# Kernel optimization log

Hardware: AMD Instinct MI355X
Metric: run time of the kernel (lower is better)

Reference implementation:

```python
import jax, jax.numpy as jnp
import numpy as np

D_MODEL = 1024
N_HEAD = 16
L, B = 2048, 2


def setup_inputs() -> dict:
    key = jax.random.key(0)
    ks = jax.random.split(key, 11)
    inp = {
        "q": jax.random.normal(ks[0], (L, B, D_MODEL), dtype=jnp.float32),
        "k": jax.random.normal(ks[1], (L, B, D_MODEL), dtype=jnp.float32),
        "v": jax.random.normal(ks[2], (L, B, D_MODEL), dtype=jnp.float32),
        "sph": jax.random.uniform(ks[3], (B, N_HEAD, L, L), dtype=jnp.float32),
        "mask": jax.random.randint(ks[4], (B, L, L), 0, 2, dtype=jnp.int32),
        # learned params (torch Linear stores W of shape [out, in]; y = x @ W.T)
        "Wq": jax.random.normal(ks[5], (D_MODEL, D_MODEL), dtype=jnp.float32) * (1.0 / np.sqrt(D_MODEL)),
        "Wk": jax.random.normal(ks[6], (D_MODEL, D_MODEL), dtype=jnp.float32) * (1.0 / np.sqrt(D_MODEL)),
        "Wv": jax.random.normal(ks[7], (D_MODEL, D_MODEL), dtype=jnp.float32) * (1.0 / np.sqrt(D_MODEL)),
        "Wfc": jax.random.normal(ks[8], (D_MODEL, D_MODEL), dtype=jnp.float32) * (1.0 / np.sqrt(D_MODEL)),
        "gamma": jnp.ones((D_MODEL,), dtype=jnp.float32),
        "beta": jnp.zeros((D_MODEL,), dtype=jnp.float32),
    }
    return inp


def reference(q, k, v, sph, mask, Wq, Wk, Wv, Wfc, gamma, beta):
    # q, k, v: [L, B, D]  ->  batch-first [B, L, D]
    n_head = N_HEAD
    Lq, Bb, D = q.shape
    d_k = D // n_head
    x_q = jnp.transpose(q, (1, 0, 2))
    x_k = jnp.transpose(k, (1, 0, 2))
    x_v = jnp.transpose(v, (1, 0, 2))
    residual = x_q  # [B, L, D]

    # projections (no bias), split heads: [B, H, L, d_k]
    qh = (x_q @ Wq.T).reshape(Bb, Lq, n_head, d_k).transpose(0, 2, 1, 3)
    kh = (x_k @ Wk.T).reshape(Bb, Lq, n_head, d_k).transpose(0, 2, 1, 3)
    vh = (x_v @ Wv.T).reshape(Bb, Lq, n_head, d_k).transpose(0, 2, 1, 3)

    scale = jnp.asarray(d_k, qh.dtype) ** 0.5
    attn = jnp.einsum('bhqd,bhkd->bhqk', qh / scale, kh)
    attn = attn * sph                                   # spatial decay modulation
    attn = jnp.where(mask[:, None, :, :] == 0, jnp.asarray(-1e9, attn.dtype), attn)
    p_attn = jax.nn.softmax(attn, axis=-1)              # dropout is identity in eval

    out = jnp.einsum('bhqk,bhkd->bhqd', p_attn, vh)     # [B, H, L, d_k]
    out = out.transpose(0, 2, 1, 3).reshape(Bb, Lq, D)
    out = out @ Wfc.T + residual                        # fc (no bias) + residual

    # LayerNorm(eps=1e-6)
    mu = jnp.mean(out, axis=-1, keepdims=True)
    var = jnp.var(out, axis=-1, keepdims=True)
    out = (out - mu) * jax.lax.rsqrt(var + 1e-6) * gamma + beta

    return jnp.transpose(out, (1, 0, 2)), p_attn
```

## Files before the change

kernel.cpp:

```cpp
#include <hip/hip_runtime.h>
#include <hip/hip_bf16.h>

#define LL 2048
#define BB 2
#define DD 1024
#define HH 16
#define DKk 64

typedef __attribute__((ext_vector_type(8))) short s8v;
typedef __attribute__((ext_vector_type(8))) unsigned short u8v;
typedef __attribute__((ext_vector_type(4))) float f4v;

__device__ __forceinline__ ushort f2b(float f){
  union { __hip_bfloat16 h; ushort u; } c; c.h = __float2bfloat16(f); return c.u;
}
__device__ __forceinline__ float b2f(ushort u){
  union { __hip_bfloat16 h; ushort u; } c; c.u = u; return __bfloat162float(c.h);
}
__device__ __forceinline__ void nts4(float* p, f4v v){ __builtin_nontemporal_store(v, (f4v*)p); }

__global__ __launch_bounds__(256) void pack_all_kernel(
    const float* __restrict__ q, const float* __restrict__ k, const float* __restrict__ v,
    const float* __restrict__ Wq, const float* __restrict__ Wk,
    const float* __restrict__ Wv, const float* __restrict__ Wfc,
    const int* __restrict__ mask,
    ushort* __restrict__ xq, ushort* __restrict__ xk, ushort* __restrict__ xv,
    ushort* __restrict__ wb, unsigned* __restrict__ mbits2){
  int blk = blockIdx.x;
  if (blk < 2048){
    int t = blk*256 + threadIdx.x;
    int m = t >> 7;
    int dc = (t & 127) << 3;
    int b = m >> 11, l = m & (LL-1);
    size_t src = ((size_t)(l*BB + b) << 10) + dc;
    size_t dst = ((size_t)m << 10) + dc;
    #pragma unroll
    for (int i=0;i<3;++i){
      const float* ss = (i==0)?q:(i==1)?k:v;
      ushort* dd = (i==0)?xq:(i==1)?xk:xv;
      float4 a = *(const float4*)(ss+src);
      float4 bb = *(const float4*)(ss+src+4);
      u8v o;
      o[0]=f2b(a.x); o[1]=f2b(a.y); o[2]=f2b(a.z); o[3]=f2b(a.w);
      o[4]=f2b(bb.x);o[5]=f2b(bb.y);o[6]=f2b(bb.z);o[7]=f2b(bb.w);
      *(u8v*)(dd+dst) = o;
    }
  } else if (blk < 4096){
    int t = (blk-2048)*256 + threadIdx.x;
    int which = t >> 17;
    size_t idx = (size_t)(t & 131071) << 3;
    const float* s = (which==0)?Wq:(which==1)?Wk:(which==2)?Wv:Wfc;
    float4 a = *(const float4*)(s+idx);
    float4 b4 = *(const float4*)(s+idx+4);
    u8v o;
    o[0]=f2b(a.x);o[1]=f2b(a.y);o[2]=f2b(a.z);o[3]=f2b(a.w);
    o[4]=f2b(b4.x);o[5]=f2b(b4.y);o[6]=f2b(b4.z);o[7]=f2b(b4.w);
    *(u8v*)(wb + ((size_t)which<<20) + idx) = o;
  } else {
    int t = (blk-4096)*256 + threadIdx.x;
    int rowg = t >> 6, lane = t & 63;
    const int* mrow = mask + ((size_t)rowg<<11) + (lane<<2);
    unsigned mw = 0;
    #pragma unroll
    for (int ct=0; ct<8; ++ct){
      int4 a = *(const int4*)(mrow + (ct<<8));
      unsigned nib = (a.x&1) | ((a.y&1)<<1) | ((a.z&1)<<2) | ((a.w&1)<<3);
      mw |= nib << (ct*4);
    }
    mbits2[((size_t)rowg<<6) + lane] = mw;
  }
}

__device__ __forceinline__ void gemm_body(
    const ushort* __restrict__ A, const ushort* __restrict__ W,
    ushort* __restrict__ outb, float* __restrict__ outf, const float* __restrict__ resid,
    int mode, float scale){
  __shared__ ushort As[4096];
  __shared__ ushort Bs[4096];
  int tid = threadIdx.x;
  int w = tid>>6, lane = tid&63, lane15 = lane&15, g = lane>>4;
  int m0 = blockIdx.y<<7, n0 = blockIdx.x<<7;
  int wr = w>>1, wc = w&1;
  f4v z4 = {0.f,0.f,0.f,0.f};
  f4v acc[4][4];
  #pragma unroll
  for (int i=0;i<4;++i)
    #pragma unroll
    for (int j=0;j<4;++j) acc[i][j] = z4;

  int f0 = tid, f1 = 256 + tid;
  int r0 = f0>>2, c0 = (f0&3)<<3;
  int r1 = f1>>2, c1 = (f1&3)<<3;
  for (int k0=0; k0<1024; k0+=32){
    *(s8v*)&As[(r0<<5)+c0] = *(const s8v*)&A[((size_t)(m0+r0)<<10) + k0 + c0];
    *(s8v*)&As[(r1<<5)+c1] = *(const s8v*)&A[((size_t)(m0+r1)<<10) + k0 + c1];
    *(s8v*)&Bs[(r0<<5)+c0] = *(const s8v*)&W[((size_t)(n0+r0)<<10) + k0 + c0];
    *(s8v*)&Bs[(r1<<5)+c1] = *(const s8v*)&W[((size_t)(n0+r1)<<10) + k0 + c1];
    __syncthreads();
    s8v af[4], bf_[4];
    #pragma unroll
    for (int mi=0;mi<4;++mi) af[mi] = *(s8v*)&As[((wr*64 + mi*16 + lane15)<<5) + (g<<3)];
    #pragma unroll
    for (int ni=0;ni<4;++ni) bf_[ni] = *(s8v*)&Bs[((wc*64 + ni*16 + lane15)<<5) + (g<<3)];
    #pragma unroll
    for (int mi=0;mi<4;++mi)
      #pragma unroll
      for (int ni=0;ni<4;++ni)
        acc[mi][ni] = __builtin_amdgcn_mfma_f32_16x16x32_bf16(af[mi], bf_[ni], acc[mi][ni], 0,0,0);
    __syncthreads();
  }
  #pragma unroll
  for (int mi=0;mi<4;++mi){
    #pragma unroll
    for (int ni=0;ni<4;++ni){
      int mbase = m0 + wr*64 + mi*16 + (g<<2);
      int ncol  = n0 + wc*64 + ni*16 + lane15;
      if (mode==0){
        int b=mbase>>11, h=ncol>>6, j=ncol&63;
        size_t o = (((size_t)(b*HH+h)*LL + (mbase&2047))<<6) + j;
        #pragma unroll
        for (int r=0;r<4;++r) outb[o + ((size_t)r<<6)] = f2b(acc[mi][ni][r]*scale);
      } else if (mode==2){
        int b=mbase>>11, h=ncol>>6, j=ncol&63;
        ushort4 pk = make_ushort4(f2b(acc[mi][ni][0]), f2b(acc[mi][ni][1]),
                                  f2b(acc[mi][ni][2]), f2b(acc[mi][ni][3]));
        *(ushort4*)&outb[(((size_t)(b*HH+h)*DKk + j)<<11) + (mbase&2047)] = pk;
      } else {
        int b=mbase>>11, l2=mbase&2047;
        #pragma unroll
        for (int r=0;r<4;++r)
          outf[((size_t)(mbase+r)<<10)+ncol] =
              acc[mi][ni][r] + resid[((size_t)((l2+r)*BB + b)<<10) + ncol];
      }
    }
  }
}

__global__ __launch_bounds__(256) void gemm_qkv_kernel(
    const ushort* __restrict__ xq, const ushort* __restrict__ xk, const ushort* __restrict__ xv,
    const ushort* __restrict__ wb, ushort* __restrict__ Qh, ushort* __restrict__ Kh, ushort* __restrict__ Vt){
  int z = blockIdx.z;
  const ushort* A = (z==0)?xq:(z==1)?xk:xv;
  const ushort* W = wb + ((size_t)z<<20);
  ushort* outb = (z==0)?Qh:(z==1)?Kh:Vt;
  int mode = (z==2)?2:0;
  float scale = (z==0)?0.125f:1.0f;
  gemm_body(A, W, outb, nullptr, nullptr, mode, scale);
}

__global__ __launch_bounds__(256) void gemm_fc_kernel(
    const ushort* __restrict__ ao, const ushort* __restrict__ wfc,
    const float* __restrict__ resid, float* __restrict__ fco){
  gemm_body(ao, wfc, nullptr, fco, resid, 3, 1.0f);
}

__global__ __launch_bounds__(1024, 4) void attn_kernel(
    const ushort* __restrict__ Qh, const ushort* __restrict__ Kh, const ushort* __restrict__ Vt,
    const float* __restrict__ sph, const unsigned* __restrict__ mbits2,
    float* __restrict__ p_out, ushort* __restrict__ attn_out){
  extern __shared__ char smem[];
  float* pbuf   = (float*)(smem + 16384);
  float* redsum = (float*)(smem + 16384 + 13056);
  int tid = threadIdx.x, w = tid>>6, lane = tid&63, lane15 = lane&15, g = lane>>4;
  int bid = blockIdx.x;
  int qt = bid & 127, h = (bid>>7)&15, b = bid>>11;
  int q0 = qt<<4;
  size_t bh = (size_t)b*HH + h;
  int qrow = q0 + w;

  const float* sph_r = sph + ((bh*LL + qrow)<<11) + (lane<<2);
  unsigned mw = mbits2[(((size_t)b*LL + qrow)<<6) + lane];

  const ushort* Qbase = Qh + ((bh*LL + q0 + lane15)<<6) + (g<<3);
  s8v qa0 = *(const s8v*)Qbase;
  s8v qa1 = *(const s8v*)(Qbase + 32);

  int rswz = (w&7)<<4;
  int aswz = (lane15&7)<<4;
  int ds = w & 3, kg = w >> 2;
  float sum = 0.f;
  f4v sp0, sp1;
  ushort4 ev[8];
  f4v oacc = {0.f,0.f,0.f,0.f};

  asm volatile("global_load_dwordx4 %0, %1, off" : "=v"(sp0) : "v"(sph_r));

  #pragma unroll
  for (int ct=0; ct<8; ++ct){
    if (ct<7){
      const float* pn = sph_r + ((ct+1)<<8);
      if (ct&1) asm volatile("global_load_dwordx4 %0, %1, off" : "=v"(sp0) : "v"(pn));
      else      asm volatile("global_load_dwordx4 %0, %1, off" : "=v"(sp1) : "v"(pn));
    }

    const ushort* Kp = Kh + ((bh*LL + (ct<<8) + (w<<4) + lane15)<<6) + (g<<3);
    s8v kb0 = *(const s8v*)Kp;
    s8v kb1 = *(const s8v*)(Kp + 32);
    f4v cacc = {0.f,0.f,0.f,0.f};
    cacc = __builtin_amdgcn_mfma_f32_16x16x32_bf16(qa0, kb0, cacc, 0,0,0);
    cacc = __builtin_amdgcn_mfma_f32_16x16x32_bf16(qa1, kb1, cacc, 0,0,0);
    char* Sb = smem + ((ct&1)<<13);
    int colb = ((w<<4) + lane15)<<1;
    #pragma unroll
    for (int r=0;r<4;++r){
      int ri = (g<<2)+r;
      *(ushort*)(Sb + (ri<<9) + (colb ^ ((ri&7)<<4))) = f2b(cacc[r]);
    }
    __syncthreads();

    f4v spv;
    if (ct&1){ asm volatile("s_waitcnt vmcnt(0)" : "+v"(sp1)); spv = sp1; }
    else     { asm volatile("s_waitcnt vmcnt(0)" : "+v"(sp0)); spv = sp0; }
    __builtin_amdgcn_sched_barrier(0);

    char* Srow = Sb + (w<<9);
    int boff = (lane<<3) ^ rswz;
    ushort4 sv = *(ushort4*)(Srow + boff);
    unsigned m4 = mw >> (ct*4);
    float e0 = (m4&1) ? __expf(b2f(sv.x)*spv[0]) : 0.f;
    float e1 = (m4&2) ? __expf(b2f(sv.y)*spv[1]) : 0.f;
    float e2 = (m4&4) ? __expf(b2f(sv.z)*spv[2]) : 0.f;
    float e3 = (m4&8) ? __expf(b2f(sv.w)*spv[3]) : 0.f;
    sum += (e0+e1)+(e2+e3);
    ushort4 eb = make_ushort4(f2b(e0), f2b(e1), f2b(e2), f2b(e3));
    ev[ct] = eb;
    *(ushort4*)(Srow + boff) = eb;
    __syncthreads();

    const ushort* Vb = Vt + ((bh*DKk + (ds<<4) + lane15)<<11) + (ct<<8) + (kg<<6) + (g<<3);
    s8v vb0 = *(const s8v*)Vb;
    s8v vb1 = *(const s8v*)(Vb + 32);
    char* Sa = Sb + (lane15<<9);
    s8v pa0 = *(s8v*)(Sa + (((kg<<7) + (g<<4)) ^ aswz));
    s8v pa1 = *(s8v*)(Sa + (((kg<<7) + 64 + (g<<4)) ^ aswz));
    oacc = __builtin_amdgcn_mfma_f32_16x16x32_bf16(pa0, vb0, oacc, 0,0,0);
    oacc = __builtin_amdgcn_mfma_f32_16x16x32_bf16(pa1, vb1, oacc, 0,0,0);
  }

  #pragma unroll
  for (int off=1; off<64; off<<=1) sum += __shfl_xor(sum, off, 64);
  if (lane==0) redsum[w] = sum;
  float inv = 1.0f / sum;
  float* prow = p_out + ((bh*LL + qrow)<<11) + (lane<<2);
  #pragma unroll
  for (int ct=0;ct<8;++ct){
    f4v o;
    o[0]=b2f(ev[ct].x)*inv; o[1]=b2f(ev[ct].y)*inv;
    o[2]=b2f(ev[ct].z)*inv; o[3]=b2f(ev[ct].w)*inv;
    nts4(prow + (ct<<8), o);
  }

  if (kg){
    float* pp = pbuf + (kg-1)*1088;
    #pragma unroll
    for (int r=0;r<4;++r) pp[((g<<2)+r)*68 + (ds<<4) + lane15] = oacc[r];
  }
  __syncthreads();
  if (kg==0){
    #pragma unroll
    for (int p3=0;p3<3;++p3){
      float* pp = pbuf + p3*1088;
      #pragma unroll
      for (int r=0;r<4;++r) oacc[r] += pp[((g<<2)+r)*68 + (ds<<4) + lane15];
    }
    #pragma unroll
    for (int r=0;r<4;++r){
      int qr = (g<<2)+r;
      float val = oacc[r] / redsum[qr];
      attn_out[((size_t)(b*LL + q0 + qr)<<10) + (h<<6) + (ds<<4) + lane15] = f2b(val);
    }
  }
}

__global__ __launch_bounds__(256) void ln_kernel(const float* __restrict__ fc,
    const float* __restrict__ gamma, const float* __restrict__ beta, float* __restrict__ out){
  __shared__ float rs[4], rq[4];
  int m = blockIdx.x, tid = threadIdx.x;
  int d0 = tid<<2;
  float4 x = *(const float4*)(fc + ((size_t)m<<10) + d0);
  float s = x.x+x.y+x.z+x.w;
  float sq = x.x*x.x+x.y*x.y+x.z*x.z+x.w*x.w;
  #pragma unroll
  for (int off=32; off; off>>=1){ s += __shfl_xor(s,off,64); sq += __shfl_xor(sq,off,64); }
  if ((tid&63)==0){ rs[tid>>6]=s; rq[tid>>6]=sq; }
  __syncthreads();
  float ts = rs[0]+rs[1]+rs[2]+rs[3];
  float tq = rq[0]+rq[1]+rq[2]+rq[3];
  float mu = ts*(1.0f/1024.0f);
  float var = tq*(1.0f/1024.0f) - mu*mu;
  float rr = rsqrtf(var + 1e-6f);
  float4 gm = *(const float4*)(gamma + d0);
  float4 bt = *(const float4*)(beta + d0);
  float4 y;
  y.x=(x.x-mu)*rr*gm.x+bt.x;
  y.y=(x.y-mu)*rr*gm.y+bt.y;
  y.z=(x.z-mu)*rr*gm.z+bt.z;
  y.w=(x.w-mu)*rr*gm.w+bt.w;
  int b=m>>11, l2=m&2047;
  *(float4*)(out + ((size_t)(l2*BB+b)<<10) + d0) = y;
}

extern "C" void kernel_launch(void* const* d_in, const int* in_sizes, int n_in,
                              void* d_out, int out_size, void* d_ws, size_t ws_size,
                              hipStream_t stream){
  const float* q    = (const float*)d_in[0];
  const float* k    = (const float*)d_in[1];
  const float* v    = (const float*)d_in[2];
  const float* sph  = (const float*)d_in[3];
  const int*   mask = (const int*)d_in[4];
  const float* Wq   = (const float*)d_in[5];
  const float* Wk   = (const float*)d_in[6];
  const float* Wv   = (const float*)d_in[7];
  const float* Wfc  = (const float*)d_in[8];
  const float* gamma= (const float*)d_in[9];
  const float* beta = (const float*)d_in[10];
  float* outp  = (float*)d_out;
  float* p_out = outp + 4194304;

  char* ws = (char*)d_ws;
  ushort* xq  = (ushort*)(ws);
  ushort* xk  = (ushort*)(ws + 8388608);
  ushort* xv  = (ushort*)(ws + 16777216);
  ushort* wb  = (ushort*)(ws + 25165824);
  ushort* Qh  = (ushort*)(ws + 33554432);
  ushort* Kh  = (ushort*)(ws + 41943040);
  ushort* Vt  = (ushort*)(ws + 50331648);
  ushort* ao  = (ushort*)(ws + 58720256);
  float*  fco = (float*)(ws + 67108864);
  unsigned* mbits2 = (unsigned*)(ws + 83886080);

  pack_all_kernel<<<5120,256,0,stream>>>(q,k,v,Wq,Wk,Wv,Wfc,mask,xq,xk,xv,wb,mbits2);
  gemm_qkv_kernel<<<dim3(8,32,3),256,0,stream>>>(xq,xk,xv,wb,Qh,Kh,Vt);
  attn_kernel<<<4096,1024,29504,stream>>>(Qh,Kh,Vt,sph,mbits2,p_out,ao);
  gemm_fc_kernel<<<dim3(8,32),256,0,stream>>>(ao, wb + 3145728, q, fco);
  ln_kernel<<<4096,256,0,stream>>>(fco, gamma, beta, outp);
}
```

Baseline: 569.0 us.

## Restructure attention into 256-thread blocks of 8 query rows

Attention blocks shrink from 1024 threads covering 16 query rows to 256 threads covering 8 rows. Each wave now computes four score tiles and owns a full 16-wide d slice of the PV product, so the cross-wave partial-sum reduction through shared memory goes away. The mask is repacked as 64-bit words with 8 consecutive bits per lane so each lane handles 8 columns. In exchange, half of each 16-row MFMA tile is wasted (only 8 real query rows), and K/V are re-read by twice as many blocks.

```diff
diff --git a/kernel.cpp b/kernel.cpp
--- a/kernel.cpp
+++ b/kernel.cpp
@@ -25,7 +25,7 @@
     const float* __restrict__ Wv, const float* __restrict__ Wfc,
     const int* __restrict__ mask,
     ushort* __restrict__ xq, ushort* __restrict__ xk, ushort* __restrict__ xv,
-    ushort* __restrict__ wb, unsigned* __restrict__ mbits2){
+    ushort* __restrict__ wb, unsigned long long* __restrict__ pmask){
   int blk = blockIdx.x;
   if (blk < 2048){
     int t = blk*256 + threadIdx.x;
@@ -58,16 +58,18 @@
     *(u8v*)(wb + ((size_t)which<<20) + idx) = o;
   } else {
     int t = (blk-4096)*256 + threadIdx.x;
-    int rowg = t >> 6, lane = t & 63;
-    const int* mrow = mask + ((size_t)rowg<<11) + (lane<<2);
-    unsigned mw = 0;
+    int rowg = t >> 5, lg = t & 31;
+    const int* mrow = mask + ((size_t)rowg<<11) + (lg<<3);
+    unsigned long long pm = 0ull;
     #pragma unroll
     for (int ct=0; ct<8; ++ct){
       int4 a = *(const int4*)(mrow + (ct<<8));
-      unsigned nib = (a.x&1) | ((a.y&1)<<1) | ((a.z&1)<<2) | ((a.w&1)<<3);
-      mw |= nib << (ct*4);
-    }
-    mbits2[((size_t)rowg<<6) + lane] = mw;
+      int4 b4 = *(const int4*)(mrow + (ct<<8) + 4);
+      unsigned by = (a.x&1)|((a.y&1)<<1)|((a.z&1)<<2)|((a.w&1)<<3)
+                  |((b4.x&1)<<4)|((b4.y&1)<<5)|((b4.z&1)<<6)|((b4.w&1)<<7);
+      pm |= (unsigned long long)by << (ct*8);
+    }
+    pmask[t] = pm;
   }
 }
 
@@ -154,120 +156,126 @@
   gemm_body(ao, wfc, nullptr, fco, resid, 3, 1.0f);
 }
 
-__global__ __launch_bounds__(1024, 4) void attn_kernel(
+__global__ __launch_bounds__(256, 4) void attn_kernel(
     const ushort* __restrict__ Qh, const ushort* __restrict__ Kh, const ushort* __restrict__ Vt,
-    const float* __restrict__ sph, const unsigned* __restrict__ mbits2,
+    const float* __restrict__ sph, const unsigned long long* __restrict__ pmask,
     float* __restrict__ p_out, ushort* __restrict__ attn_out){
   extern __shared__ char smem[];
-  float* pbuf   = (float*)(smem + 16384);
-  float* redsum = (float*)(smem + 16384 + 13056);
+  float* redsum = (float*)(smem + 8192);
   int tid = threadIdx.x, w = tid>>6, lane = tid&63, lane15 = lane&15, g = lane>>4;
   int bid = blockIdx.x;
-  int qt = bid & 127, h = (bid>>7)&15, b = bid>>11;
-  int q0 = qt<<4;
+  int qt = bid & 255, h = (bid>>8)&15, b = bid>>12;
+  int q0 = qt<<3;
   size_t bh = (size_t)b*HH + h;
-  int qrow = q0 + w;
-
-  const float* sph_r = sph + ((bh*LL + qrow)<<11) + (lane<<2);
-  unsigned mw = mbits2[(((size_t)b*LL + qrow)<<6) + lane];
-
-  const ushort* Qbase = Qh + ((bh*LL + q0 + lane15)<<6) + (g<<3);
+
+  int row = (w<<1) + (lane>>5);
+  int lg = lane & 31;
+  int qrow = q0 + row;
+  const float* sph_r = sph + ((bh*LL + qrow)<<11) + (lg<<3);
+  unsigned long long pm = pmask[(((size_t)b*LL + qrow)<<5) + lg];
+
+  const ushort* Qbase = Qh + ((bh*LL + q0 + (lane15&7))<<6) + (g<<3);
   s8v qa0 = *(const s8v*)Qbase;
   s8v qa1 = *(const s8v*)(Qbase + 32);
-
-  int rswz = (w&7)<<4;
-  int aswz = (lane15&7)<<4;
-  int ds = w & 3, kg = w >> 2;
+  const ushort* Kp = Kh + ((bh*LL + (w<<6) + lane15)<<6) + (g<<3);
+  const ushort* Vb = Vt + ((bh*DKk + (w<<4) + lane15)<<11) + (g<<3);
+
+  int rswz = row<<4;
+  int arow = lane15 & 7;
+  char* Sa0 = smem + (arow<<9);
+  int aswz = arow<<4;
+
   float sum = 0.f;
-  f4v sp0, sp1;
-  ushort4 ev[8];
+  u8v ev[8];
   f4v oacc = {0.f,0.f,0.f,0.f};
-
-  asm volatile("global_load_dwordx4 %0, %1, off" : "=v"(sp0) : "v"(sph_r));
+  f4v spA0 = *(const f4v*)(sph_r);
+  f4v spA1 = *(const f4v*)(sph_r + 4);
+  f4v spB0, spB1;
 
   #pragma unroll
   for (int ct=0; ct<8; ++ct){
+    char* Sb = smem + ((ct&1)<<12);
+    #pragma unroll
+    for (int cc=0; cc<4; ++cc){
+      const ushort* Kb = Kp + ((size_t)(ct<<14)) + (cc<<10);
+      s8v kb0 = *(const s8v*)Kb;
+      s8v kb1 = *(const s8v*)(Kb + 32);
+      f4v cacc = {0.f,0.f,0.f,0.f};
+      cacc = __builtin_amdgcn_mfma_f32_16x16x32_bf16(qa0, kb0, cacc, 0,0,0);
+      cacc = __builtin_amdgcn_mfma_f32_16x16x32_bf16(qa1, kb1, cacc, 0,0,0);
+      if (g < 2){
+        int colb = ((w<<2)+cc)<<5;
+        int cb = colb + (lane15<<1);
+        #pragma unroll
+        for (int r=0;r<4;++r){
+          int ri = (g<<2)+r;
+          *(ushort*)(Sb + (ri<<9) + (cb ^ (ri<<4))) = f2b(cacc[r]);
+        }
+      }
+    }
+    __syncthreads();
+
     if (ct<7){
       const float* pn = sph_r + ((ct+1)<<8);
-      if (ct&1) asm volatile("global_load_dwordx4 %0, %1, off" : "=v"(sp0) : "v"(pn));
-      else      asm volatile("global_load_dwordx4 %0, %1, off" : "=v"(sp1) : "v"(pn));
-    }
-
-    const ushort* Kp = Kh + ((bh*LL + (ct<<8) + (w<<4) + lane15)<<6) + (g<<3);
-    s8v kb0 = *(const s8v*)Kp;
-    s8v kb1 = *(const s8v*)(Kp + 32);
-    f4v cacc = {0.f,0.f,0.f,0.f};
-    cacc = __builtin_amdgcn_mfma_f32_16x16x32_bf16(qa0, kb0, cacc, 0,0,0);
-    cacc = __builtin_amdgcn_mfma_f32_16x16x32_bf16(qa1, kb1, cacc, 0,0,0);
-    char* Sb = smem + ((ct&1)<<13);
-    int colb = ((w<<4) + lane15)<<1;
-    #pragma unroll
-    for (int r=0;r<4;++r){
-      int ri = (g<<2)+r;
-      *(ushort*)(Sb + (ri<<9) + (colb ^ ((ri&7)<<4))) = f2b(cacc[r]);
-    }
+      if (ct&1){ spA0 = *(const f4v*)pn; spA1 = *(const f4v*)(pn+4); }
+      else     { spB0 = *(const f4v*)pn; spB1 = *(const f4v*)(pn+4); }
+    }
+    f4v s0 = (ct&1) ? spB0 : spA0;
+    f4v s1 = (ct&1) ? spB1 : spA1;
+
+    char* Srow = Sb + (row<<9);
+    int boff = (lg<<4) ^ rswz;
+    u8v sv = *(u8v*)(Srow + boff);
+    unsigned m8 = (unsigned)(pm >> (ct*8));
+    float e0 = (m8&1)   ? __expf(b2f(sv[0])*s0[0]) : 0.f;
+    float e1 = (m8&2)   ? __expf(b2f(sv[1])*s0[1]) : 0.f;
+    float e2 = (m8&4)   ? __expf(b2f(sv[2])*s0[2]) : 0.f;
+    float e3 = (m8&8)   ? __expf(b2f(sv[3])*s0[3]) : 0.f;
+    float e4 = (m8&16)  ? __expf(b2f(sv[4])*s1[0]) : 0.f;
+    float e5 = (m8&32)  ? __expf(b2f(sv[5])*s1[1]) : 0.f;
+    float e6 = (m8&64)  ? __expf(b2f(sv[6])*s1[2]) : 0.f;
+    float e7 = (m8&128) ? __expf(b2f(sv[7])*s1[3]) : 0.f;
+    sum += ((e0+e1)+(e2+e3)) + ((e4+e5)+(e6+e7));
+    u8v eb;
+    eb[0]=f2b(e0); eb[1]=f2b(e1); eb[2]=f2b(e2); eb[3]=f2b(e3);
+    eb[4]=f2b(e4); eb[5]=f2b(e5); eb[6]=f2b(e6); eb[7]=f2b(e7);
+    ev[ct] = eb;
+    *(u8v*)(Srow + boff) = eb;
     __syncthreads();
 
-    f4v spv;
-    if (ct&1){ asm volatile("s_waitcnt vmcnt(0)" : "+v"(sp1)); spv = sp1; }
-    else     { asm volatile("s_waitcnt vmcnt(0)" : "+v"(sp0)); spv = sp0; }
-    __builtin_amdgcn_sched_barrier(0);
-
-    char* Srow = Sb + (w<<9);
-    int boff = (lane<<3) ^ rswz;
-    ushort4 sv = *(ushort4*)(Srow + boff);
-    unsigned m4 = mw >> (ct*4);
-    float e0 = (m4&1) ? __expf(b2f(sv.x)*spv[0]) : 0.f;
-    float e1 = (m4&2) ? __expf(b2f(sv.y)*spv[1]) : 0.f;
-    float e2 = (m4&4) ? __expf(b2f(sv.z)*spv[2]) : 0.f;
-    float e3 = (m4&8) ? __expf(b2f(sv.w)*spv[3]) : 0.f;
-    sum += (e0+e1)+(e2+e3);
-    ushort4 eb = make_ushort4(f2b(e0), f2b(e1), f2b(e2), f2b(e3));
-    ev[ct] = eb;
-    *(ushort4*)(Srow + boff) = eb;
-    __syncthreads();
-
-    const ushort* Vb = Vt + ((bh*DKk + (ds<<4) + lane15)<<11) + (ct<<8) + (kg<<6) + (g<<3);
-    s8v vb0 = *(const s8v*)Vb;
-    s8v vb1 = *(const s8v*)(Vb + 32);
-    char* Sa = Sb + (lane15<<9);
-    s8v pa0 = *(s8v*)(Sa + (((kg<<7) + (g<<4)) ^ aswz));
-    s8v pa1 = *(s8v*)(Sa + (((kg<<7) + 64 + (g<<4)) ^ aswz));
-    oacc = __builtin_amdgcn_mfma_f32_16x16x32_bf16(pa0, vb0, oacc, 0,0,0);
-    oacc = __builtin_amdgcn_mfma_f32_16x16x32_bf16(pa1, vb1, oacc, 0,0,0);
-  }
-
-  #pragma unroll
-  for (int off=1; off<64; off<<=1) sum += __shfl_xor(sum, off, 64);
-  if (lane==0) redsum[w] = sum;
+    char* Sa = smem + ((ct&1)<<12) + (arow<<9);
+    #pragma unroll
+    for (int kk=0; kk<8; ++kk){
+      s8v pa = *(s8v*)(Sa + (((kk<<6) + (g<<4)) ^ aswz));
+      s8v vb = *(const s8v*)(Vb + (ct<<8) + (kk<<5));
+      oacc = __builtin_amdgcn_mfma_f32_16x16x32_bf16(pa, vb, oacc, 0,0,0);
+    }
+  }
+
+  #pragma unroll
+  for (int off=1; off<32; off<<=1) sum += __shfl_xor(sum, off, 64);
+  if (lg==0) redsum[row] = sum;
+  __syncthreads();
+
   float inv = 1.0f / sum;
-  float* prow = p_out + ((bh*LL + qrow)<<11) + (lane<<2);
+  float* prow = p_out + ((bh*LL + qrow)<<11) + (lg<<3);
   #pragma unroll
   for (int ct=0;ct<8;++ct){
-    f4v o;
-    o[0]=b2f(ev[ct].x)*inv; o[1]=b2f(ev[ct].y)*inv;
-    o[2]=b2f(ev[ct].z)*inv; o[3]=b2f(ev[ct].w)*inv;
-    nts4(prow + (ct<<8), o);
-  }
-
-  if (kg){
-    float* pp = pbuf + (kg-1)*1088;
-    #pragma unroll
-    for (int r=0;r<4;++r) pp[((g<<2)+r)*68 + (ds<<4) + lane15] = oacc[r];
-  }
-  __syncthreads();
-  if (kg==0){
-    #pragma unroll
-    for (int p3=0;p3<3;++p3){
-      float* pp = pbuf + p3*1088;
-      #pragma unroll
-      for (int r=0;r<4;++r) oacc[r] += pp[((g<<2)+r)*68 + (ds<<4) + lane15];
-    }
+    f4v o0, o1;
+    o0[0]=b2f(ev[ct][0])*inv; o0[1]=b2f(ev[ct][1])*inv;
+    o0[2]=b2f(ev[ct][2])*inv; o0[3]=b2f(ev[ct][3])*inv;
+    o1[0]=b2f(ev[ct][4])*inv; o1[1]=b2f(ev[ct][5])*inv;
+    o1[2]=b2f(ev[ct][6])*inv; o1[3]=b2f(ev[ct][7])*inv;
+    nts4(prow + (ct<<8), o0);
+    nts4(prow + (ct<<8) + 4, o1);
+  }
+
+  if (g < 2){
     #pragma unroll
     for (int r=0;r<4;++r){
       int qr = (g<<2)+r;
       float val = oacc[r] / redsum[qr];
-      attn_out[((size_t)(b*LL + q0 + qr)<<10) + (h<<6) + (ds<<4) + lane15] = f2b(val);
+      attn_out[((size_t)(b*LL + q0 + qr)<<10) + (h<<6) + (w<<4) + lane15] = f2b(val);
     }
   }
 }
@@ -327,11 +335,11 @@
   ushort* Vt  = (ushort*)(ws + 50331648);
   ushort* ao  = (ushort*)(ws + 58720256);
   float*  fco = (float*)(ws + 67108864);
-  unsigned* mbits2 = (unsigned*)(ws + 83886080);
-
-  pack_all_kernel<<<5120,256,0,stream>>>(q,k,v,Wq,Wk,Wv,Wfc,mask,xq,xk,xv,wb,mbits2);
+  unsigned long long* pmask = (unsigned long long*)(ws + 83886080);
+
+  pack_all_kernel<<<4608,256,0,stream>>>(q,k,v,Wq,Wk,Wv,Wfc,mask,xq,xk,xv,wb,pmask);
   gemm_qkv_kernel<<<dim3(8,32,3),256,0,stream>>>(xq,xk,xv,wb,Qh,Kh,Vt);
-  attn_kernel<<<4096,1024,29504,stream>>>(Qh,Kh,Vt,sph,mbits2,p_out,ao);
+  attn_kernel<<<8192,256,8224,stream>>>(Qh,Kh,Vt,sph,pmask,p_out,ao);
   gemm_fc_kernel<<<dim3(8,32),256,0,stream>>>(ao, wb + 3145728, q, fco);
   ln_kernel<<<4096,256,0,stream>>>(fco, gamma, beta, outp);
 }
```

Result: slower. 712.9 us (+25.3%).
